# Optimization experiments

Hardware: AMD Instinct MI355X
Metric: run time of the kernel (lower is better)

The kernel has to match this reference:

```python
import jax, jax.numpy as jnp
import numpy as np

C_S, C_P, C_H, H, P_QK, P_V = 384, 128, 16, 12, 4, 8
B, N = 1, 512
INF = 1e5
EPS = 1e-8


def quat_to_rot(q):
    w, x, y, z = q[..., 0], q[..., 1], q[..., 2], q[..., 3]
    return jnp.stack([
        jnp.stack([1 - 2 * (y * y + z * z), 2 * (x * y - w * z), 2 * (x * z + w * y)], -1),
        jnp.stack([2 * (x * y + w * z), 1 - 2 * (x * x + z * z), 2 * (y * z - w * x)], -1),
        jnp.stack([2 * (x * z - w * y), 2 * (y * z + w * x), 1 - 2 * (x * x + y * y)], -1),
    ], -2)


def layer_norm(x, g, b):
    m = x.mean(-1, keepdims=True)
    v = ((x - m) ** 2).mean(-1, keepdims=True)
    return (x - m) * jax.lax.rsqrt(v + 1e-5) * g + b


def setup_inputs():
    key = jax.random.key(0)
    ks = iter(jax.random.split(key, 64))

    def w(shape, scale=0.02):
        return jax.random.normal(next(ks), shape, dtype=jnp.float32) * scale

    inp = {}
    inp['s'] = jax.random.normal(next(ks), (B, N, C_S), dtype=jnp.float32)
    inp['p'] = jax.random.normal(next(ks), (B, N, N, C_P), dtype=jnp.float32)
    q = jax.random.normal(next(ks), (B, N, 4), dtype=jnp.float32)
    inp['rot'] = quat_to_rot(q / jnp.linalg.norm(q, axis=-1, keepdims=True))
    inp['trans'] = jax.random.normal(next(ks), (B, N, 3), dtype=jnp.float32)
    inp['mask'] = jnp.ones((B, N), dtype=jnp.float32)
    inp['w_q'] = w((C_S, H * C_H)); inp['b_q'] = jnp.zeros((H * C_H,), jnp.float32)
    inp['w_kv'] = w((C_S, 2 * H * C_H)); inp['b_kv'] = jnp.zeros((2 * H * C_H,), jnp.float32)
    inp['w_qp'] = w((C_S, H * P_QK * 3)); inp['b_qp'] = jnp.zeros((H * P_QK * 3,), jnp.float32)
    inp['w_kvp'] = w((C_S, H * (P_QK + P_V) * 3)); inp['b_kvp'] = jnp.zeros((H * (P_QK + P_V) * 3,), jnp.float32)
    inp['w_b'] = w((C_P, H)); inp['b_b'] = jnp.zeros((H,), jnp.float32)
    inp['head_w'] = w((H,), 0.5)
    d_out = H * (C_H + C_P + P_V * 4)  # 2112
    inp['w_o'] = w((d_out, C_S)); inp['b_o'] = jnp.zeros((C_S,), jnp.float32)
    inp['ln1_g'] = jnp.ones((C_S,), jnp.float32); inp['ln1_b'] = jnp.zeros((C_S,), jnp.float32)
    for i in (1, 2, 3):
        inp['tw%d' % i] = w((C_S, C_S)); inp['tb%d' % i] = jnp.zeros((C_S,), jnp.float32)
    inp['ln2_g'] = jnp.ones((C_S,), jnp.float32); inp['ln2_b'] = jnp.zeros((C_S,), jnp.float32)
    inp['bb_w'] = w((C_S, 6)); inp['bb_b'] = jnp.zeros((6,), jnp.float32)
    return inp


def forward(s, p, rot, trans, mask, w_q, b_q, w_kv, b_kv, w_qp, b_qp, w_kvp, b_kvp,
            w_b, b_b, head_w, w_o, b_o, ln1_g, ln1_b,
            tw1, tb1, tw2, tb2, tw3, tb3, ln2_g, ln2_b, bb_w, bb_b):
    # ---- Invariant Point Attention ----
    q = (s @ w_q + b_q).reshape(B, N, H, C_H)
    k, v = jnp.split((s @ w_kv + b_kv).reshape(B, N, H, 2 * C_H), 2, axis=-1)
    qp = (s @ w_qp + b_qp).reshape(B, N, H * P_QK, 3)
    qp = (jnp.einsum('bnij,bnpj->bnpi', rot, qp) + trans[:, :, None, :]).reshape(B, N, H, P_QK, 3)
    kvp = (s @ w_kvp + b_kvp).reshape(B, N, H * (P_QK + P_V), 3)
    kvp = (jnp.einsum('bnij,bnpj->bnpi', rot, kvp) + trans[:, :, None, :]).reshape(B, N, H, P_QK + P_V, 3)
    kp, vp = kvp[..., :P_QK, :], kvp[..., P_QK:, :]
    bias = p @ w_b + b_b  # [B,N,N,H]
    a = jnp.einsum('bihc,bjhc->bhij', q, k) * float(np.sqrt(1.0 / (3 * C_H)))
    a = a + float(np.sqrt(1.0 / 3)) * jnp.transpose(bias, (0, 3, 1, 2))
    d2 = ((qp[:, :, None] - kp[:, None]) ** 2).sum(-1)  # [B,N,N,H,Pqk]
    hw = jax.nn.softplus(head_w) * float(np.sqrt(1.0 / (3 * (P_QK * 9.0 / 2))))
    pt_att = -0.5 * (d2 * hw[:, None]).sum(-1)  # [B,N,N,H]
    sq_mask = (mask[:, :, None] * mask[:, None, :] - 1.0) * INF  # [B,N,N]
    a = jax.nn.softmax(a + jnp.transpose(pt_att, (0, 3, 1, 2)) + sq_mask[:, None], axis=-1)
    o = jnp.einsum('bhij,bjhc->bihc', a, v).reshape(B, N, H * C_H)
    op = jnp.einsum('bhij,bjhpc->bihpc', a, vp) - trans[:, :, None, None, :]
    op = jnp.einsum('bnji,bnhpj->bnhpi', rot, op)  # invert-apply frames
    op_norm = jnp.sqrt((op ** 2).sum(-1) + EPS)  # [B,N,H,Pv]
    o_pair = jnp.einsum('bhij,bijc->bihc', a, p).reshape(B, N, H * C_P)
    cat = jnp.concatenate([o, op.reshape(B, N, H * P_V * 3), op_norm.reshape(B, N, H * P_V), o_pair], -1)
    s = s + cat @ w_o + b_o
    s = layer_norm(s, ln1_g, ln1_b)
    # ---- structure transition (1 layer, residual + LN) ----
    h = jax.nn.relu(s @ tw1 + tb1)
    h = jax.nn.relu(h @ tw2 + tb2)
    s = layer_norm(s + h @ tw3 + tb3, ln2_g, ln2_b)
    # ---- backbone update + frame compose ----
    upd = s @ bb_w + bb_b  # [B,N,6]
    quat = jnp.concatenate([jnp.ones((B, N, 1), s.dtype), upd[..., :3]], -1)
    quat = quat / jnp.linalg.norm(quat, axis=-1, keepdims=True)
    r_u = quat_to_rot(quat)
    rot_new = jnp.einsum('bnij,bnjk->bnik', rot, r_u)
    trans_new = jnp.einsum('bnij,bnj->bni', rot, upd[..., 3:]) + trans
    return s, rot_new, trans_new


def reference(s, p, rot, trans, mask, w_q, b_q, w_kv, b_kv, w_qp, b_qp, w_kvp, b_kvp,
              w_b, b_b, head_w, w_o, b_o, ln1_g, ln1_b,
              tw1, tb1, tw2, tb2, tw3, tb3, ln2_g, ln2_b, bb_w, bb_b):
    return forward(s, p, rot, trans, mask, w_q, b_q, w_kv, b_kv, w_qp, b_qp, w_kvp, b_kvp,
                   w_b, b_b, head_w, w_o, b_o, ln1_g, ln1_b,
                   tw1, tb1, tw2, tb2, tw3, tb3, ln2_g, ln2_b, bb_w, bb_b)
```

## Files before the change

### kernel.cpp

```cpp
#include <hip/hip_runtime.h>
#include <math.h>

#define N 512
#define CS 384
#define CP 128
#define CH 16
#define NH 12
#define NN (N*N)
#define DCAT 2112
#define INFV 100000.0f

__device__ __constant__ float SC_QK = 0.14433756729740643f;
#define SC_B  0.57735026918962576f
#define HW_SC 0.13608276348795434f

typedef __attribute__((ext_vector_type(8))) short bf16x8;
typedef __attribute__((ext_vector_type(4))) float f32x4;
typedef __attribute__((ext_vector_type(4))) short sh4;
typedef __attribute__((ext_vector_type(4))) unsigned u32x4;
typedef unsigned short ushort_t;

__device__ inline short f2bf(float v) {
    unsigned u = __builtin_bit_cast(unsigned, v);
    u += 0x7FFF + ((u >> 16) & 1);
    return (short)(u >> 16);
}
__device__ inline float bf2f(ushort_t u) {
    unsigned x = ((unsigned)u) << 16;
    return __builtin_bit_cast(float, x);
}
__device__ __forceinline__ unsigned cvtpk(float a, float b) {
    unsigned r;
    asm("v_cvt_pk_bf16_f32 %0, %1, %2" : "=v"(r) : "v"(a), "v"(b));
    return r;
}

__device__ __forceinline__ void gload16(const void* g, void* l) {
    __builtin_amdgcn_global_load_lds(
        (const __attribute__((address_space(1))) unsigned int*)g,
        (__attribute__((address_space(3))) unsigned int*)l,
        16, 0, 0);
}

struct FrontArgs {
    const float* wsrc0; const float* wsrc1; const float* wsrc2; const float* wsrc3;
    const float* wsrc4; const float* wsrc5; const float* wsrc6; const float* wsrc7;
    ushort_t* wdst0; ushort_t* wdst1; ushort_t* wdst2; ushort_t* wdst3;
    ushort_t* wdst4; ushort_t* wdst5; ushort_t* wdst6; ushort_t* wdst7;
    const float* s; ushort_t* sbf;
    const float* bq; const float* bkv; const float* bqp; const float* bkvp;
    float* biasp;
    const float* p; const float* w_b; const float* b_b; ushort_t* bias_b;
};

__global__ __launch_bounds__(256) void front_kernel(FrontArgs a)
{
    __shared__ __align__(16) char SM[36864];
    const int b = blockIdx.x;
    const int t = threadIdx.x;
    if (b < 4096) {
        float* Pf = (float*)SM;
        ushort_t* Wbs = (ushort_t*)(SM + 32768);
        const int w = t >> 6;
        const size_t row0 = (size_t)b * 64;

        for (int idx = t; idx < 2048; idx += 256) {
            int h = idx >> 7, c = idx & 127;
            float v = (h < 12) ? a.w_b[c * 12 + h] : 0.f;
            int byte = h * 256 + ((c * 2) ^ ((h & 7) << 4));
            *(ushort_t*)((char*)Wbs + byte) = (ushort_t)f2bf(v);
        }
        #pragma unroll
        for (int k = 0; k < 8; ++k) {
            int s2 = k * 256 + t;
            int row = s2 >> 5, ch = s2 & 31;
            const char* src = (const char*)(a.p + (row0 + row) * 128) + ((ch ^ (row & 7)) * 16);
            gload16(src, (char*)Pf + (size_t)(k * 256 + w * 64) * 16);
        }
        __syncthreads();

        const int l = t & 63, lr = l & 15, hk = l >> 4;
        const int jb = w * 16;
        f32x4 acc = (f32x4){0.f, 0.f, 0.f, 0.f};
        #pragma unroll
        for (int ks = 0; ks < 4; ++ks) {
            int row = jb + lr;
            int kc = ks * 8 + hk * 2;
            const char* base = (const char*)Pf + row * 512;
            f32x4 v0 = *(const f32x4*)(base + ((kc ^ (row & 7)) * 16));
            f32x4 v1 = *(const f32x4*)(base + (((kc + 1) ^ (row & 7)) * 16));
            bf16x8 afr;
            afr[0] = f2bf(v0[0]); afr[1] = f2bf(v0[1]); afr[2] = f2bf(v0[2]); afr[3] = f2bf(v0[3]);
            afr[4] = f2bf(v1[0]); afr[5] = f2bf(v1[1]); afr[6] = f2bf(v1[2]); afr[7] = f2bf(v1[3]);
            bf16x8 bfr = *(const bf16x8*)((char*)Wbs + lr * 256 +
                            ((ks * 64 + hk * 16) ^ ((lr & 7) << 4)));
            acc = __builtin_amdgcn_mfma_f32_16x16x32_bf16(afr, bfr, acc, 0, 0, 0);
        }
        if (lr < 12) {
            float bb = a.b_b[lr];
            size_t gj = row0 + jb + hk * 4;
            sh4 o;
            #pragma unroll
            for (int r = 0; r < 4; ++r) o[r] = f2bf(SC_B * (acc[r] + bb));
            *(sh4*)(a.bias_b + (size_t)lr * NN + gj) = o;
        }
    } else {
        const int bp = b - 4096;
        if (bp < 1668) {
            const float* src; ushort_t* dst; int begin, nx, Nc, K;
            if      (bp < 72)   { src=a.wsrc0; dst=a.wdst0; begin=0;    nx=6;  Nc=192; K=384; }
            else if (bp < 216)  { src=a.wsrc1; dst=a.wdst1; begin=72;   nx=12; Nc=384; K=384; }
            else if (bp < 276)  { src=a.wsrc2; dst=a.wdst2; begin=216;  nx=5;  Nc=144; K=384; }
            else if (bp < 444)  { src=a.wsrc3; dst=a.wdst3; begin=276;  nx=14; Nc=432; K=384; }
            else if (bp < 1236) { src=a.wsrc4; dst=a.wdst4; begin=444;  nx=12; Nc=384; K=2112; }
            else if (bp < 1380) { src=a.wsrc5; dst=a.wdst5; begin=1236; nx=12; Nc=384; K=384; }
            else if (bp < 1524) { src=a.wsrc6; dst=a.wdst6; begin=1380; nx=12; Nc=384; K=384; }
            else                { src=a.wsrc7; dst=a.wdst7; begin=1524; nx=12; Nc=384; K=384; }
            int lb = bp - begin;
            int cx = (lb % nx) * 32, ky = (lb / nx) * 32;
            float (*tile)[33] = (float(*)[33])SM;
            const int tx = t & 31, ty = t >> 5;
            for (int r = ty; r < 32; r += 8) {
                int c = cx + tx;
                tile[r][tx] = (c < Nc) ? src[(size_t)(ky + r) * Nc + c] : 0.f;
            }
            __syncthreads();
            for (int r = ty; r < 32; r += 8) {
                int orow = cx + r;
                if (orow < Nc)
                    dst[(size_t)orow * K + ky + tx] = (ushort_t)f2bf(tile[tx][r]);
            }
        } else if (bp < 1860) {
            int i4 = (bp - 1668) * 256 + t;
            f32x4 v = *(const f32x4*)(a.s + (size_t)i4 * 4);
            sh4 o;
            o[0] = f2bf(v[0]); o[1] = f2bf(v[1]); o[2] = f2bf(v[2]); o[3] = f2bf(v[3]);
            *(sh4*)(a.sbf + (size_t)i4 * 4) = o;
        } else {
            for (int idx = t; idx < 1152; idx += 256) {
                float v;
                if (idx < 192)      v = a.bq[idx];
                else if (idx < 576) v = a.bkv[idx - 192];
                else if (idx < 720) v = a.bqp[idx - 576];
                else                v = a.bkvp[idx - 720];
                a.biasp[idx] = v;
            }
        }
    }
}

__global__ __launch_bounds__(256) void gemm_bf16(
    const ushort_t* __restrict__ A, const ushort_t* __restrict__ Bt,
    float* __restrict__ part, int K, int KOUT, int nk)
{
    __shared__ __align__(16) ushort_t As[2][2048];
    __shared__ __align__(16) ushort_t Bs[2][2048];
    const int t = threadIdx.x, w = t >> 6, l = t & 63;
    const int i0 = blockIdx.x * 64, n0 = blockIdx.y * 64, sp = blockIdx.z;
    const int kbase = sp * nk * 32;

    const int srow = w * 16 + (l >> 2);
    const int skb = (l & 3) ^ ((srow >> 1) & 3);
    const ushort_t* aSrc = A + (size_t)(i0 + srow) * K + kbase + skb * 8;
    const ushort_t* bSrc = Bt + (size_t)(n0 + srow) * K + kbase + skb * 8;
    ushort_t* aDst = &As[0][0] + w * 512;
    ushort_t* bDst = &Bs[0][0] + w * 512;

    const int r0 = (w >> 1) * 32, c0 = (w & 1) * 32, lr = l & 15, hk = l >> 4;
    int aOff[2], bOff[2];
    #pragma unroll
    for (int m = 0; m < 2; ++m) {
        int row = r0 + m * 16 + lr;
        aOff[m] = row * 64 + ((hk ^ ((row >> 1) & 3)) << 4);
    }
    #pragma unroll
    for (int n = 0; n < 2; ++n) {
        int row = c0 + n * 16 + lr;
        bOff[n] = row * 64 + ((hk ^ ((row >> 1) & 3)) << 4);
    }

    f32x4 acc[2][2];
    #pragma unroll
    for (int m = 0; m < 2; ++m)
        #pragma unroll
        for (int n = 0; n < 2; ++n) acc[m][n] = (f32x4){0.f, 0.f, 0.f, 0.f};

    gload16(aSrc, aDst);
    gload16(bSrc, bDst);
    __syncthreads();

    int cur = 0;
    for (int it = 0; it < nk; ++it) {
        if (it + 1 < nk) {
            gload16(aSrc + (it + 1) * 32, aDst + (cur ^ 1) * 2048);
            gload16(bSrc + (it + 1) * 32, bDst + (cur ^ 1) * 2048);
        }
        const char* ab = (const char*)&As[cur][0];
        const char* bb = (const char*)&Bs[cur][0];
        bf16x8 a0 = *(const bf16x8*)(ab + aOff[0]);
// ... 207 lines not shown
    __shared__ float buf[1152];
    __shared__ float hwv[12], kc28[12];
    const int j = blockIdx.x, t = threadIdx.x;
    for (int c = t; c < 1152; c += 256)
        buf[c] = biasp[c] + parts[(size_t)j * 1152 + c] + parts[(size_t)(512 + j) * 1152 + c];
    if (t >= 192 && t < 204) {
        int h = t - 192;
        hwv[h] = HW_SC * log1pf(expf(head_w[h]));
    }
    __syncthreads();
    if (t < 192) {
        int base = 576 + t * 3;
        const float* R = rot + j * 9;
        const float* T = trans + j * 3;
        float x = buf[base], y = buf[base + 1], z = buf[base + 2];
        float nx = R[0]*x + R[1]*y + R[2]*z + T[0];
        float ny = R[3]*x + R[4]*y + R[5]*z + T[1];
        float nz = R[6]*x + R[7]*y + R[8]*z + T[2];
        buf[base] = nx; buf[base + 1] = ny; buf[base + 2] = nz;
    }
    __syncthreads();
    if (t < 12) {
        float s2 = 0.f;
        #pragma unroll
        for (int e = 0; e < 12; ++e) { float v = buf[720 + t * 36 + e]; s2 += v * v; }
        kc28[t] = -0.5f * hwv[t] * s2 + (mask[j] - 1.0f) * INFV;
    }
    __syncthreads();
    if (t < 192) {
        int h = t >> 4, c0 = (t & 15) * 2;
        float hwf = hwv[h];
        #pragma unroll
        for (int e = 0; e < 2; ++e) {
            int c = c0 + e;
            float qv, kv2;
            if (c < 16)      { qv = SC_QK * buf[h * 16 + c];           kv2 = buf[192 + h * 32 + c]; }
            else if (c < 28) { qv = hwf * buf[576 + h * 12 + (c - 16)]; kv2 = buf[720 + h * 36 + (c - 16)]; }
            else if (c == 28){ qv = 1.f;                               kv2 = kc28[h]; }
            else             { qv = 0.f;                               kv2 = 0.f; }
            Qext[(size_t)h * 16384 + j * 32 + c] = (ushort_t)f2bf(qv);
            Kext[(size_t)h * 16384 + j * 32 + c] = (ushort_t)f2bf(kv2);
        }
    }
    for (int idx = t; idx < 576; idx += 256) {
        int h = idx / 48, c = idx % 48;
        float v;
        if (c < 16)      v = buf[192 + h * 32 + 16 + c];
        else if (c < 40) v = buf[720 + h * 36 + 12 + (c - 16)];
        else             v = 0.f;
        Vext[(size_t)h * 24576 + c * 512 + j] = (ushort_t)f2bf(v);
    }
}

__global__ __launch_bounds__(256) void attn_mfma(
    const ushort_t* __restrict__ Qext, const ushort_t* __restrict__ Kext,
    const ushort_t* __restrict__ bias_b, const ushort_t* __restrict__ Vext,
    const float* __restrict__ rot, const float* __restrict__ trans,
    ushort_t* __restrict__ attn_b, ushort_t* __restrict__ catb)
{
    __shared__ float sc[16 * 516];
    __shared__ float redm[64];
    __shared__ float invr[16];
    __shared__ float opl[16][25];
    const int t = threadIdx.x, w = t >> 6, l = t & 63;
    const int i0 = blockIdx.x * 16, h = blockIdx.y;
    const int lr = l & 15, hk = l >> 4;

    #pragma unroll
    for (int it = 0; it < 8; ++it) {
        int elem = (t + it * 256) * 4;
        int i = elem >> 9, j = elem & 511;
        sh4 raw = *(const sh4*)(bias_b + (size_t)h * NN + (size_t)(i0 + i) * 512 + j);
        f32x4 v;
        v[0] = bf2f((ushort_t)raw[0]); v[1] = bf2f((ushort_t)raw[1]);
        v[2] = bf2f((ushort_t)raw[2]); v[3] = bf2f((ushort_t)raw[3]);
        *(f32x4*)(sc + i * 516 + j) = v;
    }
    __syncthreads();

    bf16x8 a0 = *(const bf16x8*)(Qext + (size_t)h * 16384 + (i0 + lr) * 32 + hk * 8);
    f32x4 acc[8];
    #pragma unroll
    for (int n = 0; n < 8; ++n) {
        bf16x8 b = *(const bf16x8*)(Kext + (size_t)h * 16384 +
                                    (w * 128 + n * 16 + lr) * 32 + hk * 8);
        acc[n] = __builtin_amdgcn_mfma_f32_16x16x32_bf16(a0, b, (f32x4){0.f,0.f,0.f,0.f}, 0, 0, 0);
    }

    float rmax[4] = {-3.0e38f, -3.0e38f, -3.0e38f, -3.0e38f};
    #pragma unroll
    for (int n = 0; n < 8; ++n) {
        int col = w * 128 + n * 16 + lr;
        #pragma unroll
        for (int r = 0; r < 4; ++r) {
            int row = hk * 4 + r;
            float v = acc[n][r] + sc[row * 516 + col];
            sc[row * 516 + col] = v;
            rmax[r] = fmaxf(rmax[r], v);
        }
    }
    #pragma unroll
    for (int r = 0; r < 4; ++r) {
        float v = rmax[r];
        v = fmaxf(v, __shfl_xor(v, 1));
        v = fmaxf(v, __shfl_xor(v, 2));
        v = fmaxf(v, __shfl_xor(v, 4));
        v = fmaxf(v, __shfl_xor(v, 8));
        if (lr == 0) redm[w * 16 + hk * 4 + r] = v;
    }
    __syncthreads();

    {
        int row = t >> 4, g = t & 15;
        float mx = fmaxf(fmaxf(redm[row], redm[16 + row]),
                         fmaxf(redm[32 + row], redm[48 + row]));
        float sum = 0.f;
        float* sr = sc + row * 516;
        for (int c = g; c < 512; c += 16) {
            float e = expf(sr[c] - mx);
            sr[c] = e;
            sum += e;
        }
        sum += __shfl_xor(sum, 1);
        sum += __shfl_xor(sum, 2);
        sum += __shfl_xor(sum, 4);
        sum += __shfl_xor(sum, 8);
        if (g == 0) invr[row] = 1.0f / sum;
    }
    __syncthreads();

    #pragma unroll
    for (int it = 0; it < 8; ++it) {
        int elem = (t + it * 256) * 4;
        int i = elem >> 9, j = elem & 511;
        f32x4 v = *(const f32x4*)(sc + i * 516 + j);
        float iv = invr[i];
        sh4 o;
        o[0] = f2bf(v[0] * iv); o[1] = f2bf(v[1] * iv);
        o[2] = f2bf(v[2] * iv); o[3] = f2bf(v[3] * iv);
        *(sh4*)(attn_b + (size_t)h * NN + (size_t)(i0 + i) * 512 + j) = o;
    }

    f32x4 acc3[3];
    acc3[0] = (f32x4){0.f,0.f,0.f,0.f};
    acc3[1] = (f32x4){0.f,0.f,0.f,0.f};
    acc3[2] = (f32x4){0.f,0.f,0.f,0.f};
    const ushort_t* vbase = Vext + (size_t)h * 24576 + lr * 512 + hk * 8;
    #pragma unroll
    for (int kt = 0; kt < 16; ++kt) {
        const float* srow = sc + lr * 516 + kt * 32 + hk * 8;
        f32x4 x0 = *(const f32x4*)(srow);
        f32x4 x1 = *(const f32x4*)(srow + 4);
        u32x4 ap;
        ap[0] = cvtpk(x0[0], x0[1]); ap[1] = cvtpk(x0[2], x0[3]);
        ap[2] = cvtpk(x1[0], x1[1]); ap[3] = cvtpk(x1[2], x1[3]);
        bf16x8 af = __builtin_bit_cast(bf16x8, ap);
        #pragma unroll
        for (int n = 0; n < 3; ++n) {
            bf16x8 bf = *(const bf16x8*)(vbase + n * 16 * 512 + kt * 32);
            acc3[n] = __builtin_amdgcn_mfma_f32_16x16x32_bf16(af, bf, acc3[n], 0, 0, 0);
        }
    }
    #pragma unroll
    for (int n = 0; n < 3; ++n) {
        int c = n * 16 + lr;
        #pragma unroll
        for (int r = 0; r < 4; ++r) {
            int ri = hk * 4 + r;
            float val = acc3[n][r] * invr[ri];
            if (c < 16)
                catb[(size_t)(i0 + ri) * DCAT + h * 16 + c] = (ushort_t)f2bf(val);
            else if (c < 40)
                opl[ri][c - 16] = val;
        }
    }
    __syncthreads();
    if (t < 128) {
        int i16 = t >> 3, pv = t & 7;
        int i = i0 + i16;
        const float* T = trans + i * 3;
        const float* R = rot + i * 9;
        float x = opl[i16][pv * 3 + 0] - T[0];
        float y = opl[i16][pv * 3 + 1] - T[1];
        float z = opl[i16][pv * 3 + 2] - T[2];
        float rx = R[0] * x + R[3] * y + R[6] * z;
        float ry = R[1] * x + R[4] * y + R[7] * z;
        float rz = R[2] * x + R[5] * y + R[8] * z;
        float nm = sqrtf(rx * rx + ry * ry + rz * rz + 1e-8f);
        ushort_t* cr = catb + (size_t)i * DCAT;
        cr[192 + h * 24 + pv * 3 + 0] = (ushort_t)f2bf(rx);
        cr[192 + h * 24 + pv * 3 + 1] = (ushort_t)f2bf(ry);
        cr[192 + h * 24 + pv * 3 + 2] = (ushort_t)f2bf(rz);
        cr[480 + h * 8 + pv] = (ushort_t)f2bf(nm);
    }
}

__global__ __launch_bounds__(256) void opair_mfma(
    const ushort_t* __restrict__ attn_b, const float* __restrict__ p,
    ushort_t* __restrict__ catb)
{
    __shared__ __align__(16) ushort_t As2[16 * 512];
    __shared__ __align__(16) ushort_t Pt[2][128 * 72];
    const int t = threadIdx.x, i = blockIdx.x;
    const int w = t >> 6, l = t & 63;
    const int lr = l & 15, hk = l >> 4;

    #pragma unroll
    for (int ii = 0; ii < 4; ++ii) {
        int idx = (t + ii * 256) * 8;
        int h = idx >> 9, j = idx & 511;
        bf16x8 v;
        if (h < 12) v = *(const bf16x8*)(attn_b + (size_t)h * NN + (size_t)i * 512 + j);
        else        v = (bf16x8){0,0,0,0,0,0,0,0};
        *(bf16x8*)((char*)As2 + h * 1024 + ((j * 2) ^ ((h & 7) << 4))) = v;
    }

    const int jA = (t >> 3) * 2;
    const int c0 = (t & 7) * 16;
    const float* psrc = p + (size_t)i * 65536;

    f32x4 va[4], vb[4];
    #pragma unroll
    for (int q = 0; q < 4; ++q) {
        va[q] = *(const f32x4*)(psrc + (size_t)jA * 128 + c0 + q * 4);
        vb[q] = *(const f32x4*)(psrc + (size_t)(jA + 1) * 128 + c0 + q * 4);
    }

    #define PACK_TILE(buf)                                                       \
        {                                                                        \
            ushort_t* ptw = &Pt[buf][0];                                         \
            _Pragma("unroll")                                                    \
            for (int e = 0; e < 16; ++e) {                                       \
                int c = c0 + e;                                                  \
                unsigned pk = cvtpk(va[e >> 2][e & 3], vb[e >> 2][e & 3]);       \
                int byte = c * 144 + ((jA * 2) ^ (((c >> 4) & 7) << 4));         \
                *(unsigned*)((char*)ptw + byte) = pk;                            \
            }                                                                    \
        }
    #define LOAD_TILE(tile)                                                      \
        {                                                                        \
            const float* s0 = psrc + (size_t)((tile) * 64 + jA) * 128 + c0;      \
            _Pragma("unroll")                                                    \
            for (int q = 0; q < 4; ++q) {                                        \
                va[q] = *(const f32x4*)(s0 + q * 4);                             \
                vb[q] = *(const f32x4*)(s0 + 128 + q * 4);                       \
            }                                                                    \
        }

    PACK_TILE(0);
    LOAD_TILE(1);

    f32x4 acc[2];
    acc[0] = (f32x4){0.f, 0.f, 0.f, 0.f};
    acc[1] = (f32x4){0.f, 0.f, 0.f, 0.f};

    int cur = 0;
    for (int tile = 0; tile < 8; ++tile) {
        __syncthreads();
        const char* pt = (const char*)&Pt[cur][0];
        #pragma unroll
        for (int ks = 0; ks < 2; ++ks) {
            bf16x8 afr = *(const bf16x8*)((char*)As2 + lr * 1024 +
                            ((tile * 128 + ks * 64 + hk * 16) ^ ((lr & 7) << 4)));
            #pragma unroll
            for (int n = 0; n < 2; ++n) {
                int c = w * 32 + n * 16 + lr;
                bf16x8 bfr = *(const bf16x8*)(pt + c * 144 +
                                ((ks * 64 + hk * 16) ^ (((c >> 4) & 7) << 4)));
                acc[n] = __builtin_amdgcn_mfma_f32_16x16x32_bf16(afr, bfr, acc[n], 0, 0, 0);
            }
        }
        if (tile < 7) {
            PACK_TILE(cur ^ 1);
            if (tile < 6) LOAD_TILE(tile + 2);
            cur ^= 1;
        }
    }
    #undef PACK_TILE
    #undef LOAD_TILE
    #pragma unroll
    for (int n = 0; n < 2; ++n) {
        int c = w * 32 + n * 16 + lr;
        #pragma unroll
        for (int r = 0; r < 4; ++r) {
            int h = hk * 4 + r;
            if (h < 12)
                catb[(size_t)i * DCAT + 576 + h * 128 + c] = (ushort_t)f2bf(acc[n][r]);
        }
    }
}

extern "C" void kernel_launch(void* const* d_in, const int* in_sizes, int n_in,
                              void* d_out, int out_size, void* d_ws, size_t ws_size,
                              hipStream_t stream)
{
    const float* s      = (const float*)d_in[0];
    const float* p      = (const float*)d_in[1];
    const float* rot    = (const float*)d_in[2];
    const float* trans  = (const float*)d_in[3];
    const float* mask   = (const float*)d_in[4];
    const float* w_q    = (const float*)d_in[5];
    const float* b_q    = (const float*)d_in[6];
    const float* w_kv   = (const float*)d_in[7];
    const float* b_kv   = (const float*)d_in[8];
    const float* w_qp   = (const float*)d_in[9];
    const float* b_qp   = (const float*)d_in[10];
    const float* w_kvp  = (const float*)d_in[11];
    const float* b_kvp  = (const float*)d_in[12];
    const float* w_b    = (const float*)d_in[13];
    const float* b_b    = (const float*)d_in[14];
    const float* head_w = (const float*)d_in[15];
    const float* w_o    = (const float*)d_in[16];
    const float* b_o    = (const float*)d_in[17];
    const float* ln1_g  = (const float*)d_in[18];
    const float* ln1_b  = (const float*)d_in[19];
    const float* tw1    = (const float*)d_in[20];
    const float* tb1    = (const float*)d_in[21];
    const float* tw2    = (const float*)d_in[22];
    const float* tb2    = (const float*)d_in[23];
    const float* tw3    = (const float*)d_in[24];
    const float* tb3    = (const float*)d_in[25];
    const float* ln2_g  = (const float*)d_in[26];
    const float* ln2_b  = (const float*)d_in[27];
    const float* bb_w   = (const float*)d_in[28];
    const float* bb_b   = (const float*)d_in[29];

    float* ws = (float*)d_ws;
    float*    parts  = ws;
    float*    partsB = parts + 589824;
    float*    s1     = parts + 1179648;
    float*    biasp  = s1 + 196608;
    ushort_t* ub     = (ushort_t*)(biasp + 1152);
    ushort_t* bias_b = ub;
    ushort_t* attn_b = bias_b + 3145728;
    ushort_t* catb   = attn_b + 3145728;
    ushort_t* sbf    = catb + 1081344;
    ushort_t* s1bf   = sbf + 196608;
    ushort_t* h1bf   = s1bf + 196608;
    ushort_t* h2bf   = h1bf + 196608;
    ushort_t* Qext   = h2bf + 196608;
    ushort_t* Kext   = Qext + 196608;
    ushort_t* Vext   = Kext + 196608;
    ushort_t* Wtp    = Vext + 294912;
    ushort_t* Wto    = Wtp + 442368;
    ushort_t* Wt1    = Wto + 811008;
    ushort_t* Wt2    = Wt1 + 147456;
    ushort_t* Wt3    = Wt2 + 147456;

    float* out_s     = (float*)d_out;
    float* out_rot   = out_s + 196608;
    float* out_trans = out_rot + 4608;

    FrontArgs fa;
    fa.wsrc0 = w_q;  fa.wdst0 = Wtp;
    fa.wsrc1 = w_kv; fa.wdst1 = Wtp + (size_t)192 * 384;
    fa.wsrc2 = w_qp; fa.wdst2 = Wtp + (size_t)576 * 384;
    fa.wsrc3 = w_kvp; fa.wdst3 = Wtp + (size_t)720 * 384;
    fa.wsrc4 = w_o;  fa.wdst4 = Wto;
    fa.wsrc5 = tw1;  fa.wdst5 = Wt1;
    fa.wsrc6 = tw2;  fa.wdst6 = Wt2;
    fa.wsrc7 = tw3;  fa.wdst7 = Wt3;
    fa.s = s; fa.sbf = sbf;
    fa.bq = b_q; fa.bkv = b_kv; fa.bqp = b_qp; fa.bkvp = b_kvp;
    fa.biasp = biasp;
    fa.p = p; fa.w_b = w_b; fa.b_b = b_b; fa.bias_b = bias_b;
    front_kernel<<<5957, 256, 0, stream>>>(fa);

    gemm_bf16<<<dim3(8, 18, 2), 256, 0, stream>>>(sbf, Wtp, parts, 384, 1152, 6);
    postproj_kernel<<<512, 256, 0, stream>>>(parts, biasp, rot, trans, head_w, mask,
                                             Qext, Kext, Vext);

    attn_mfma<<<dim3(32, 12), 256, 0, stream>>>(Qext, Kext, bias_b, Vext, rot, trans,
                                                attn_b, catb);
    opair_mfma<<<512, 256, 0, stream>>>(attn_b, p, catb);

    gemm_bf16<<<dim3(8, 6, 6), 256, 0, stream>>>(catb, Wto, parts, 2112, 384, 11);
    reduce_ln<<<512, 128, 0, stream>>>(parts, 6, b_o, s, ln1_g, ln1_b, s1, s1bf,
                                       nullptr, nullptr, nullptr, nullptr, nullptr, nullptr);

    gemm_bf16<<<dim3(8, 6, 3), 256, 0, stream>>>(s1bf, Wt1, parts, 384, 384, 4);
    gemm_red<<<dim3(8, 6, 3), 256, 0, stream>>>(parts, tb1, Wt2, partsB, 4);
    gemm_red<<<dim3(8, 6, 3), 256, 0, stream>>>(partsB, tb2, Wt3, parts, 4);
    reduce_ln<<<512, 128, 0, stream>>>(parts, 3, tb3, s1, ln2_g, ln2_b, out_s, nullptr,
                                       bb_w, bb_b, rot, trans, out_rot, out_trans);
}
```

Measured before the change: 124.7 us.

## Fuse pair-bias projection, softmax, and pair-output into one pass over p

The pair tensor p used to be read twice: once in the front kernel to build the pair bias and once in the opair kernel for the output-pair product. A new per-row mega_attn kernel now loads each p tile once, computes the bias by MFMA, adds precomputed QK logits, runs an online softmax across 8 tiles, and accumulates the attention-weighted sum of p in the same pass. The QK logits are now computed by a separate small kernel and written head-interleaved, and the attention-times-V product moves into its own ov_mfma kernel. This roughly halves traffic on the large p tensor and drops the bf16 bias buffer, in exchange for more synchronisation per tile and an extra kernel launch.

```diff
diff --git a/kernel.cpp b/kernel.cpp
--- a/kernel.cpp
+++ b/kernel.cpp
@@ -42,7 +42,7 @@
         16, 0, 0);
 }
 
-struct FrontArgs {
+struct PrepArgs {
     const float* wsrc0; const float* wsrc1; const float* wsrc2; const float* wsrc3;
     const float* wsrc4; const float* wsrc5; const float* wsrc6; const float* wsrc7;
     ushort_t* wdst0; ushort_t* wdst1; ushort_t* wdst2; ushort_t* wdst3;
@@ -50,101 +50,50 @@
     const float* s; ushort_t* sbf;
     const float* bq; const float* bkv; const float* bqp; const float* bkvp;
     float* biasp;
-    const float* p; const float* w_b; const float* b_b; ushort_t* bias_b;
 };
 
-__global__ __launch_bounds__(256) void front_kernel(FrontArgs a)
-{
-    __shared__ __align__(16) char SM[36864];
-    const int b = blockIdx.x;
+__global__ __launch_bounds__(256) void prep_kernel(PrepArgs a)
+{
+    __shared__ float tile[32][33];
+    const int bp = blockIdx.x;
     const int t = threadIdx.x;
-    if (b < 4096) {
-        float* Pf = (float*)SM;
-        ushort_t* Wbs = (ushort_t*)(SM + 32768);
-        const int w = t >> 6;
-        const size_t row0 = (size_t)b * 64;
-
-        for (int idx = t; idx < 2048; idx += 256) {
-            int h = idx >> 7, c = idx & 127;
-            float v = (h < 12) ? a.w_b[c * 12 + h] : 0.f;
-            int byte = h * 256 + ((c * 2) ^ ((h & 7) << 4));
-            *(ushort_t*)((char*)Wbs + byte) = (ushort_t)f2bf(v);
-        }
-        #pragma unroll
-        for (int k = 0; k < 8; ++k) {
-            int s2 = k * 256 + t;
-            int row = s2 >> 5, ch = s2 & 31;
-            const char* src = (const char*)(a.p + (row0 + row) * 128) + ((ch ^ (row & 7)) * 16);
-            gload16(src, (char*)Pf + (size_t)(k * 256 + w * 64) * 16);
+    if (bp < 1668) {
+        const float* src; ushort_t* dst; int begin, nx, Nc, K;
+        if      (bp < 72)   { src=a.wsrc0; dst=a.wdst0; begin=0;    nx=6;  Nc=192; K=384; }
+        else if (bp < 216)  { src=a.wsrc1; dst=a.wdst1; begin=72;   nx=12; Nc=384; K=384; }
+        else if (bp < 276)  { src=a.wsrc2; dst=a.wdst2; begin=216;  nx=5;  Nc=144; K=384; }
+        else if (bp < 444)  { src=a.wsrc3; dst=a.wdst3; begin=276;  nx=14; Nc=432; K=384; }
+        else if (bp < 1236) { src=a.wsrc4; dst=a.wdst4; begin=444;  nx=12; Nc=384; K=2112; }
+        else if (bp < 1380) { src=a.wsrc5; dst=a.wdst5; begin=1236; nx=12; Nc=384; K=384; }
+        else if (bp < 1524) { src=a.wsrc6; dst=a.wdst6; begin=1380; nx=12; Nc=384; K=384; }
+        else                { src=a.wsrc7; dst=a.wdst7; begin=1524; nx=12; Nc=384; K=384; }
+        int lb = bp - begin;
+        int cx = (lb % nx) * 32, ky = (lb / nx) * 32;
+        const int tx = t & 31, ty = t >> 5;
+        for (int r = ty; r < 32; r += 8) {
+            int c = cx + tx;
+            tile[r][tx] = (c < Nc) ? src[(size_t)(ky + r) * Nc + c] : 0.f;
         }
         __syncthreads();
-
-        const int l = t & 63, lr = l & 15, hk = l >> 4;
-        const int jb = w * 16;
-        f32x4 acc = (f32x4){0.f, 0.f, 0.f, 0.f};
-        #pragma unroll
-        for (int ks = 0; ks < 4; ++ks) {
-            int row = jb + lr;
-            int kc = ks * 8 + hk * 2;
-            const char* base = (const char*)Pf + row * 512;
-            f32x4 v0 = *(const f32x4*)(base + ((kc ^ (row & 7)) * 16));
-            f32x4 v1 = *(const f32x4*)(base + (((kc + 1) ^ (row & 7)) * 16));
-            bf16x8 afr;
-            afr[0] = f2bf(v0[0]); afr[1] = f2bf(v0[1]); afr[2] = f2bf(v0[2]); afr[3] = f2bf(v0[3]);
-            afr[4] = f2bf(v1[0]); afr[5] = f2bf(v1[1]); afr[6] = f2bf(v1[2]); afr[7] = f2bf(v1[3]);
-            bf16x8 bfr = *(const bf16x8*)((char*)Wbs + lr * 256 +
-                            ((ks * 64 + hk * 16) ^ ((lr & 7) << 4)));
-            acc = __builtin_amdgcn_mfma_f32_16x16x32_bf16(afr, bfr, acc, 0, 0, 0);
-        }
-        if (lr < 12) {
-            float bb = a.b_b[lr];
-            size_t gj = row0 + jb + hk * 4;
-            sh4 o;
-            #pragma unroll
-            for (int r = 0; r < 4; ++r) o[r] = f2bf(SC_B * (acc[r] + bb));
-            *(sh4*)(a.bias_b + (size_t)lr * NN + gj) = o;
-        }
+        for (int r = ty; r < 32; r += 8) {
+            int orow = cx + r;
+            if (orow < Nc)
+                dst[(size_t)orow * K + ky + tx] = (ushort_t)f2bf(tile[tx][r]);
+        }
+    } else if (bp < 1860) {
+        int i4 = (bp - 1668) * 256 + t;
+        f32x4 v = *(const f32x4*)(a.s + (size_t)i4 * 4);
+        sh4 o;
+        o[0] = f2bf(v[0]); o[1] = f2bf(v[1]); o[2] = f2bf(v[2]); o[3] = f2bf(v[3]);
+        *(sh4*)(a.sbf + (size_t)i4 * 4) = o;
     } else {
-        const int bp = b - 4096;
-        if (bp < 1668) {
-            const float* src; ushort_t* dst; int begin, nx, Nc, K;
-            if      (bp < 72)   { src=a.wsrc0; dst=a.wdst0; begin=0;    nx=6;  Nc=192; K=384; }
-            else if (bp < 216)  { src=a.wsrc1; dst=a.wdst1; begin=72;   nx=12; Nc=384; K=384; }
-            else if (bp < 276)  { src=a.wsrc2; dst=a.wdst2; begin=216;  nx=5;  Nc=144; K=384; }
-            else if (bp < 444)  { src=a.wsrc3; dst=a.wdst3; begin=276;  nx=14; Nc=432; K=384; }
-            else if (bp < 1236) { src=a.wsrc4; dst=a.wdst4; begin=444;  nx=12; Nc=384; K=2112; }
-            else if (bp < 1380) { src=a.wsrc5; dst=a.wdst5; begin=1236; nx=12; Nc=384; K=384; }
-            else if (bp < 1524) { src=a.wsrc6; dst=a.wdst6; begin=1380; nx=12; Nc=384; K=384; }
-            else                { src=a.wsrc7; dst=a.wdst7; begin=1524; nx=12; Nc=384; K=384; }
-            int lb = bp - begin;
-            int cx = (lb % nx) * 32, ky = (lb / nx) * 32;
-            float (*tile)[33] = (float(*)[33])SM;
-            const int tx = t & 31, ty = t >> 5;
-            for (int r = ty; r < 32; r += 8) {
-                int c = cx + tx;
-                tile[r][tx] = (c < Nc) ? src[(size_t)(ky + r) * Nc + c] : 0.f;
-            }
-            __syncthreads();
-            for (int r = ty; r < 32; r += 8) {
-                int orow = cx + r;
-                if (orow < Nc)
-                    dst[(size_t)orow * K + ky + tx] = (ushort_t)f2bf(tile[tx][r]);
-            }
-        } else if (bp < 1860) {
-            int i4 = (bp - 1668) * 256 + t;
-            f32x4 v = *(const f32x4*)(a.s + (size_t)i4 * 4);
-            sh4 o;
-            o[0] = f2bf(v[0]); o[1] = f2bf(v[1]); o[2] = f2bf(v[2]); o[3] = f2bf(v[3]);
-            *(sh4*)(a.sbf + (size_t)i4 * 4) = o;
-        } else {
-            for (int idx = t; idx < 1152; idx += 256) {
-                float v;
-                if (idx < 192)      v = a.bq[idx];
-                else if (idx < 576) v = a.bkv[idx - 192];
-                else if (idx < 720) v = a.bqp[idx - 576];
-                else                v = a.bkvp[idx - 720];
-                a.biasp[idx] = v;
-            }
+        for (int idx = t; idx < 1152; idx += 256) {
+            float v;
+            if (idx < 192)      v = a.bq[idx];
+            else if (idx < 576) v = a.bkv[idx - 192];
+            else if (idx < 720) v = a.bqp[idx - 576];
+            else                v = a.bkvp[idx - 720];
+            a.biasp[idx] = v;
         }
     }
 }
@@ -458,113 +407,245 @@
     }
 }
 
-__global__ __launch_bounds__(256) void attn_mfma(
+__global__ __launch_bounds__(256) void qk_kernel(
     const ushort_t* __restrict__ Qext, const ushort_t* __restrict__ Kext,
-    const ushort_t* __restrict__ bias_b, const ushort_t* __restrict__ Vext,
-    const float* __restrict__ rot, const float* __restrict__ trans,
-    ushort_t* __restrict__ attn_b, ushort_t* __restrict__ catb)
-{
-    __shared__ float sc[16 * 516];
-    __shared__ float redm[64];
-    __shared__ float invr[16];
-    __shared__ float opl[16][25];
+    ushort_t* __restrict__ qk_b)
+{
     const int t = threadIdx.x, w = t >> 6, l = t & 63;
     const int i0 = blockIdx.x * 16, h = blockIdx.y;
     const int lr = l & 15, hk = l >> 4;
-
-    #pragma unroll
-    for (int it = 0; it < 8; ++it) {
-        int elem = (t + it * 256) * 4;
-        int i = elem >> 9, j = elem & 511;
-        sh4 raw = *(const sh4*)(bias_b + (size_t)h * NN + (size_t)(i0 + i) * 512 + j);
-        f32x4 v;
-        v[0] = bf2f((ushort_t)raw[0]); v[1] = bf2f((ushort_t)raw[1]);
-        v[2] = bf2f((ushort_t)raw[2]); v[3] = bf2f((ushort_t)raw[3]);
-        *(f32x4*)(sc + i * 516 + j) = v;
-    }
-    __syncthreads();
-
     bf16x8 a0 = *(const bf16x8*)(Qext + (size_t)h * 16384 + (i0 + lr) * 32 + hk * 8);
-    f32x4 acc[8];
     #pragma unroll
     for (int n = 0; n < 8; ++n) {
         bf16x8 b = *(const bf16x8*)(Kext + (size_t)h * 16384 +
                                     (w * 128 + n * 16 + lr) * 32 + hk * 8);
-        acc[n] = __builtin_amdgcn_mfma_f32_16x16x32_bf16(a0, b, (f32x4){0.f,0.f,0.f,0.f}, 0, 0, 0);
-    }
-
-    float rmax[4] = {-3.0e38f, -3.0e38f, -3.0e38f, -3.0e38f};
-    #pragma unroll
-    for (int n = 0; n < 8; ++n) {
-        int col = w * 128 + n * 16 + lr;
+        f32x4 acc = __builtin_amdgcn_mfma_f32_16x16x32_bf16(
+                        a0, b, (f32x4){0.f, 0.f, 0.f, 0.f}, 0, 0, 0);
+        int j = w * 128 + n * 16 + lr;
         #pragma unroll
         for (int r = 0; r < 4; ++r) {
-            int row = hk * 4 + r;
-            float v = acc[n][r] + sc[row * 516 + col];
-            sc[row * 516 + col] = v;
-            rmax[r] = fmaxf(rmax[r], v);
-        }
-    }
-    #pragma unroll
-    for (int r = 0; r < 4; ++r) {
-        float v = rmax[r];
-        v = fmaxf(v, __shfl_xor(v, 1));
-        v = fmaxf(v, __shfl_xor(v, 2));
-        v = fmaxf(v, __shfl_xor(v, 4));
-        v = fmaxf(v, __shfl_xor(v, 8));
-        if (lr == 0) redm[w * 16 + hk * 4 + r] = v;
-    }
-    __syncthreads();
-
+            int i = i0 + hk * 4 + r;
+            qk_b[((size_t)i * 512 + j) * 16 + h] = (ushort_t)f2bf(acc[r]);
+        }
+    }
+}
+
+__global__ __launch_bounds__(256) void mega_attn(
+    const float* __restrict__ p, const ushort_t* __restrict__ qk_b,
+    const float* __restrict__ w_b, const float* __restrict__ b_b,
+    ushort_t* __restrict__ attn_b, ushort_t* __restrict__ catb)
+{
+    __shared__ __align__(16) ushort_t Wbs[16 * 128];
+    __shared__ __align__(16) ushort_t Pr[64 * 128];
+    __shared__ __align__(16) ushort_t Pt[128 * 72];
+    __shared__ __align__(16) ushort_t qkT[64 * 16];
+    __shared__ __align__(16) ushort_t wT[16 * 64];
+    __shared__ __align__(16) ushort_t wFull[16 * 512];
+    __shared__ float mTile[16][8];
+    __shared__ float redw[4][16], redw2[4][16];
+    __shared__ float fArr[16], lArr[16], mArr[16];
+
+    const int t = threadIdx.x, i = blockIdx.x;
+    const int w = t >> 6, l = t & 63, lr = l & 15, hk = l >> 4;
+
+    for (int idx = t; idx < 2048; idx += 256) {
+        int h = idx >> 7, c = idx & 127;
+        float v = (h < 12) ? SC_B * w_b[c * 12 + h] : 0.f;
+        *(ushort_t*)((char*)Wbs + h * 256 + ((c * 2) ^ ((h & 7) << 4))) = (ushort_t)f2bf(v);
+    }
+    const float sc_bb = (lr < 12) ? SC_B * b_b[lr] : 0.f;
+
+    const float* psrc = p + (size_t)i * 65536;
+    const int jA = (t >> 3) * 2, c0 = (t & 7) * 16;
+
+    f32x4 va[4], vb[4];
+    #define LOAD_REGS(tile)                                                      \
+        {                                                                        \
+            const float* s0 = psrc + (size_t)((tile) * 64 + jA) * 128 + c0;      \
+            _Pragma("unroll")                                                    \
+            for (int q = 0; q < 4; ++q) {                                        \
+                va[q] = *(const f32x4*)(s0 + q * 4);                             \
+                vb[q] = *(const f32x4*)(s0 + 128 + q * 4);                       \
+            }                                                                    \
+        }
+    #define WRITE_BUFS()                                                         \
+        {                                                                        \
+            _Pragma("unroll")                                                    \
+            for (int r2 = 0; r2 < 2; ++r2) {                                     \
+                int j = jA + r2;                                                 \
+                const f32x4* vr = r2 ? vb : va;                                  \
+                _Pragma("unroll")                                                \
+                for (int half = 0; half < 2; ++half) {                           \
+                    u32x4 pk;                                                    \
+                    pk[0] = cvtpk(vr[half*2][0], vr[half*2][1]);                 \
+                    pk[1] = cvtpk(vr[half*2][2], vr[half*2][3]);                 \
+                    pk[2] = cvtpk(vr[half*2+1][0], vr[half*2+1][1]);             \
+                    pk[3] = cvtpk(vr[half*2+1][2], vr[half*2+1][3]);             \
+                    int byte = j * 256 + (((c0 + half * 8) * 2) ^ ((j & 7) << 4));\
+                    *(u32x4*)((char*)Pr + byte) = pk;                            \
+                }                                                                \
+            }                                                                    \
+            _Pragma("unroll")                                                    \
+            for (int e = 0; e < 16; ++e) {                                       \
+                int c = c0 + e;                                                  \
+                unsigned pk = cvtpk(va[e >> 2][e & 3], vb[e >> 2][e & 3]);       \
+                int byte = c * 144 + ((jA * 2) ^ (((c >> 4) & 7) << 4));         \
+                *(unsigned*)((char*)Pt + byte) = pk;                             \
+            }                                                                    \
+        }
+    #define STAGE_QK(tile)                                                      \
+        if (t < 128)                                                            \
+            gload16(qk_b + ((size_t)i * 512 + (tile) * 64) * 16 + t * 8,        \
+                    (char*)qkT + t * 16);
+
+    LOAD_REGS(0);
+    STAGE_QK(0);
+    __syncthreads();
+    WRITE_BUFS();
+    LOAD_REGS(1);
+    float m_reg = -3.0e38f, l_reg = 0.f;
+    f32x4 accP[2];
+    accP[0] = (f32x4){0.f, 0.f, 0.f, 0.f};
+    accP[1] = (f32x4){0.f, 0.f, 0.f, 0.f};
+    __syncthreads();
+
+    const int jl2 = w * 16 + lr;
+    for (int tile = 0; tile < 8; ++tile) {
+        f32x4 S = (f32x4){0.f, 0.f, 0.f, 0.f};
+        #pragma unroll
+        for (int ks = 0; ks < 4; ++ks) {
+            bf16x8 afr = *(const bf16x8*)((char*)Pr + jl2 * 256 +
+                            ((ks * 64 + hk * 16) ^ ((jl2 & 7) << 4)));
+            bf16x8 bfr = *(const bf16x8*)((char*)Wbs + lr * 256 +
+                            ((ks * 64 + hk * 16) ^ ((lr & 7) << 4)));
+            S = __builtin_amdgcn_mfma_f32_16x16x32_bf16(afr, bfr, S, 0, 0, 0);
+        }
+        float sv[4];
+        float tmax = -3.0e38f;
+        #pragma unroll
+        for (int r = 0; r < 4; ++r) {
+            int jloc = w * 16 + hk * 4 + r;
+            float qkv = (lr < 12) ? bf2f(qkT[jloc * 16 + lr]) : 0.f;
+            sv[r] = S[r] + sc_bb + qkv;
+            tmax = fmaxf(tmax, sv[r]);
+        }
+        tmax = fmaxf(tmax, __shfl_xor(tmax, 16));
+        tmax = fmaxf(tmax, __shfl_xor(tmax, 32));
+        if (hk == 0) redw[w][lr] = tmax;
+        __syncthreads();
+        if (tile < 7) STAGE_QK(tile + 1);
+        float mt = fmaxf(fmaxf(redw[0][lr], redw[1][lr]),
+                         fmaxf(redw[2][lr], redw[3][lr]));
+        float m_new = fmaxf(m_reg, mt);
+        float f = __expf(m_reg - m_new);
+        m_reg = m_new;
+        float tsum = 0.f;
+        ushort_t wv16[4];
+        #pragma unroll
+        for (int r = 0; r < 4; ++r) {
+            float wv = __expf(sv[r] - m_new);
+            tsum += wv;
+            wv16[r] = (ushort_t)f2bf(wv);
+        }
+        tsum += __shfl_xor(tsum, 16);
+        tsum += __shfl_xor(tsum, 32);
+        if (hk == 0) redw2[w][lr] = tsum;
+        if (w == 0 && hk == 0) { fArr[lr] = f; mTile[lr][tile] = m_new; }
+        #pragma unroll
+        for (int r = 0; r < 4; ++r) {
+            int j = w * 16 + hk * 4 + r;
+            *(ushort_t*)((char*)wT + lr * 128 + ((j * 2) ^ ((lr & 7) << 4))) = wv16[r];
+            int jg = tile * 64 + j;
+            *(ushort_t*)((char*)wFull + lr * 1024 + ((jg * 2) ^ ((lr & 7) << 4))) = wv16[r];
+        }
+        __syncthreads();
+        float sumAll = redw2[0][lr] + redw2[1][lr] + redw2[2][lr] + redw2[3][lr];
+        l_reg = l_reg * f + sumAll;
+        #pragma unroll
+        for (int n = 0; n < 2; ++n)
+            #pragma unroll
+            for (int r = 0; r < 4; ++r) accP[n][r] *= fArr[hk * 4 + r];
+        #pragma unroll
+        for (int ks = 0; ks < 2; ++ks) {
+            bf16x8 afr = *(const bf16x8*)((char*)wT + lr * 128 +
+                            ((ks * 64 + hk * 16) ^ ((lr & 7) << 4)));
+            #pragma unroll
+            for (int n = 0; n < 2; ++n) {
+                int c = w * 32 + n * 16 + lr;
+                bf16x8 bfr = *(const bf16x8*)((char*)Pt + c * 144 +
+                                ((ks * 64 + hk * 16) ^ (((c >> 4) & 7) << 4)));
+                accP[n] = __builtin_amdgcn_mfma_f32_16x16x32_bf16(afr, bfr, accP[n], 0, 0, 0);
+            }
+        }
+        __syncthreads();
+        if (tile < 7) {
+            WRITE_BUFS();
+            if (tile < 6) LOAD_REGS(tile + 2);
+        }
+        __syncthreads();
+    }
+    #undef LOAD_REGS
+    #undef WRITE_BUFS
+    #undef STAGE_QK
+
+    if (w == 0 && hk == 0) { lArr[lr] = l_reg; mArr[lr] = m_reg; }
+    __syncthreads();
+
+    #pragma unroll
+    for (int n = 0; n < 2; ++n) {
+        int c = w * 32 + n * 16 + lr;
+        #pragma unroll
+        for (int r = 0; r < 4; ++r) {
+            int h = hk * 4 + r;
+            if (h < 12)
+                catb[(size_t)i * DCAT + 576 + h * 128 + c] =
+                    (ushort_t)f2bf(accP[n][r] / lArr[h]);
+        }
+    }
     {
-        int row = t >> 4, g = t & 15;
-        float mx = fmaxf(fmaxf(redm[row], redm[16 + row]),
-                         fmaxf(redm[32 + row], redm[48 + row]));
-        float sum = 0.f;
-        float* sr = sc + row * 516;
-        for (int c = g; c < 512; c += 16) {
-            float e = expf(sr[c] - mx);
-            sr[c] = e;
-            sum += e;
-        }
-        sum += __shfl_xor(sum, 1);
-        sum += __shfl_xor(sum, 2);
-        sum += __shfl_xor(sum, 4);
-        sum += __shfl_xor(sum, 8);
-        if (g == 0) invr[row] = 1.0f / sum;
-    }
-    __syncthreads();
-
-    #pragma unroll
-    for (int it = 0; it < 8; ++it) {
-        int elem = (t + it * 256) * 4;
-        int i = elem >> 9, j = elem & 511;
-        f32x4 v = *(const f32x4*)(sc + i * 516 + j);
-        float iv = invr[i];
-        sh4 o;
-        o[0] = f2bf(v[0] * iv); o[1] = f2bf(v[1] * iv);
-        o[2] = f2bf(v[2] * iv); o[3] = f2bf(v[3] * iv);
-        *(sh4*)(attn_b + (size_t)h * NN + (size_t)(i0 + i) * 512 + j) = o;
-    }
-
-    f32x4 acc3[3];
-    acc3[0] = (f32x4){0.f,0.f,0.f,0.f};
-    acc3[1] = (f32x4){0.f,0.f,0.f,0.f};
-    acc3[2] = (f32x4){0.f,0.f,0.f,0.f};
+        int h = t >> 4;
+        if (h < 12) {
+            float linv = 1.0f / lArr[h];
+            float mfin = mArr[h];
+            #pragma unroll
+            for (int e = 0; e < 4; ++e) {
+                int cp = (t & 15) * 4 + e;
+                int jc = cp ^ (h & 7);
+                int j0 = jc * 8;
+                float corr = __expf(mTile[h][j0 >> 6] - mfin) * linv;
+                bf16x8 raw = *(const bf16x8*)((char*)wFull + h * 1024 + cp * 16);
+                bf16x8 o;
+                #pragma unroll
+                for (int q = 0; q < 8; ++q)
+                    o[q] = (short)f2bf(bf2f((ushort_t)raw[q]) * corr);
+                *(bf16x8*)(attn_b + (size_t)h * NN + (size_t)i * 512 + j0) = o;
+            }
+        }
+    }
+}
+
+__global__ __launch_bounds__(64) void ov_mfma(
+    const ushort_t* __restrict__ attn_b, const ushort_t* __restrict__ Vext,
+    const float* __restrict__ rot, const float* __restrict__ trans,
+    ushort_t* __restrict__ catb)
+{
+    __shared__ float opl[16][25];
+    const int l = threadIdx.x;
+    const int i0 = blockIdx.x * 16, h = blockIdx.y;
+    const int lr = l & 15, hk = l >> 4;
+    f32x4 acc[3];
+    acc[0] = (f32x4){0.f,0.f,0.f,0.f};
+    acc[1] = (f32x4){0.f,0.f,0.f,0.f};
+    acc[2] = (f32x4){0.f,0.f,0.f,0.f};
+    const ushort_t* arow = attn_b + (size_t)h * NN + (size_t)(i0 + lr) * 512 + hk * 8;
     const ushort_t* vbase = Vext + (size_t)h * 24576 + lr * 512 + hk * 8;
     #pragma unroll
     for (int kt = 0; kt < 16; ++kt) {
-        const float* srow = sc + lr * 516 + kt * 32 + hk * 8;
-        f32x4 x0 = *(const f32x4*)(srow);
-        f32x4 x1 = *(const f32x4*)(srow + 4);
-        u32x4 ap;
-        ap[0] = cvtpk(x0[0], x0[1]); ap[1] = cvtpk(x0[2], x0[3]);
-        ap[2] = cvtpk(x1[0], x1[1]); ap[3] = cvtpk(x1[2], x1[3]);
-        bf16x8 af = __builtin_bit_cast(bf16x8, ap);
+        bf16x8 af = *(const bf16x8*)(arow + kt * 32);
         #pragma unroll
         for (int n = 0; n < 3; ++n) {
             bf16x8 bf = *(const bf16x8*)(vbase + n * 16 * 512 + kt * 32);
-            acc3[n] = __builtin_amdgcn_mfma_f32_16x16x32_bf16(af, bf, acc3[n], 0, 0, 0);
+            acc[n] = __builtin_amdgcn_mfma_f32_16x16x32_bf16(af, bf, acc[n], 0, 0, 0);
         }
     }
     #pragma unroll
@@ -573,16 +654,17 @@
         #pragma unroll
         for (int r = 0; r < 4; ++r) {
             int ri = hk * 4 + r;
-            float val = acc3[n][r] * invr[ri];
             if (c < 16)
-                catb[(size_t)(i0 + ri) * DCAT + h * 16 + c] = (ushort_t)f2bf(val);
+                catb[(size_t)(i0 + ri) * DCAT + h * 16 + c] = (ushort_t)f2bf(acc[n][r]);
             else if (c < 40)
-                opl[ri][c - 16] = val;
-        }
-    }
-    __syncthreads();
-    if (t < 128) {
-        int i16 = t >> 3, pv = t & 7;
+                opl[ri][c - 16] = acc[n][r];
+        }
+    }
+    __syncthreads();
+    #pragma unroll
+    for (int e = 0; e < 2; ++e) {
+        int pt = l + e * 64;
+        int i16 = pt >> 3, pv = pt & 7;
         int i = i0 + i16;
         const float* T = trans + i * 3;
         const float* R = rot + i * 9;
@@ -598,101 +680,6 @@
         cr[192 + h * 24 + pv * 3 + 1] = (ushort_t)f2bf(ry);
         cr[192 + h * 24 + pv * 3 + 2] = (ushort_t)f2bf(rz);
         cr[480 + h * 8 + pv] = (ushort_t)f2bf(nm);
-    }
-}
-
-__global__ __launch_bounds__(256) void opair_mfma(
-    const ushort_t* __restrict__ attn_b, const float* __restrict__ p,
-    ushort_t* __restrict__ catb)
-{
-    __shared__ __align__(16) ushort_t As2[16 * 512];
-    __shared__ __align__(16) ushort_t Pt[2][128 * 72];
-    const int t = threadIdx.x, i = blockIdx.x;
-    const int w = t >> 6, l = t & 63;
-    const int lr = l & 15, hk = l >> 4;
-
-    #pragma unroll
-    for (int ii = 0; ii < 4; ++ii) {
-        int idx = (t + ii * 256) * 8;
-        int h = idx >> 9, j = idx & 511;
-        bf16x8 v;
-        if (h < 12) v = *(const bf16x8*)(attn_b + (size_t)h * NN + (size_t)i * 512 + j);
-        else        v = (bf16x8){0,0,0,0,0,0,0,0};
-        *(bf16x8*)((char*)As2 + h * 1024 + ((j * 2) ^ ((h & 7) << 4))) = v;
-    }
-
-    const int jA = (t >> 3) * 2;
-    const int c0 = (t & 7) * 16;
-    const float* psrc = p + (size_t)i * 65536;
-
-    f32x4 va[4], vb[4];
-    #pragma unroll
-    for (int q = 0; q < 4; ++q) {
-        va[q] = *(const f32x4*)(psrc + (size_t)jA * 128 + c0 + q * 4);
-        vb[q] = *(const f32x4*)(psrc + (size_t)(jA + 1) * 128 + c0 + q * 4);
-    }
-
-    #define PACK_TILE(buf)                                                       \
-        {                                                                        \
-            ushort_t* ptw = &Pt[buf][0];                                         \
-            _Pragma("unroll")                                                    \
-            for (int e = 0; e < 16; ++e) {                                       \
-                int c = c0 + e;                                                  \
-                unsigned pk = cvtpk(va[e >> 2][e & 3], vb[e >> 2][e & 3]);       \
-                int byte = c * 144 + ((jA * 2) ^ (((c >> 4) & 7) << 4));         \
-                *(unsigned*)((char*)ptw + byte) = pk;                            \
-            }                                                                    \
-        }
-    #define LOAD_TILE(tile)                                                      \
-        {                                                                        \
-            const float* s0 = psrc + (size_t)((tile) * 64 + jA) * 128 + c0;      \
-            _Pragma("unroll")                                                    \
-            for (int q = 0; q < 4; ++q) {                                        \
-                va[q] = *(const f32x4*)(s0 + q * 4);                             \
-                vb[q] = *(const f32x4*)(s0 + 128 + q * 4);                       \
-            }                                                                    \
-        }
-
-    PACK_TILE(0);
-    LOAD_TILE(1);
-
-    f32x4 acc[2];
-    acc[0] = (f32x4){0.f, 0.f, 0.f, 0.f};
-    acc[1] = (f32x4){0.f, 0.f, 0.f, 0.f};
-
-    int cur = 0;
-    for (int tile = 0; tile < 8; ++tile) {
-        __syncthreads();
-        const char* pt = (const char*)&Pt[cur][0];
-        #pragma unroll
-        for (int ks = 0; ks < 2; ++ks) {
-            bf16x8 afr = *(const bf16x8*)((char*)As2 + lr * 1024 +
-                            ((tile * 128 + ks * 64 + hk * 16) ^ ((lr & 7) << 4)));
-            #pragma unroll
-            for (int n = 0; n < 2; ++n) {
-                int c = w * 32 + n * 16 + lr;
-                bf16x8 bfr = *(const bf16x8*)(pt + c * 144 +
-                                ((ks * 64 + hk * 16) ^ (((c >> 4) & 7) << 4)));
-                acc[n] = __builtin_amdgcn_mfma_f32_16x16x32_bf16(afr, bfr, acc[n], 0, 0, 0);
-            }
-        }
-        if (tile < 7) {
-            PACK_TILE(cur ^ 1);
-            if (tile < 6) LOAD_TILE(tile + 2);
-            cur ^= 1;
-        }
-    }
-    #undef PACK_TILE
-    #undef LOAD_TILE
-    #pragma unroll
-    for (int n = 0; n < 2; ++n) {
-        int c = w * 32 + n * 16 + lr;
-        #pragma unroll
-        for (int r = 0; r < 4; ++r) {
-            int h = hk * 4 + r;
-            if (h < 12)
-                catb[(size_t)i * DCAT + 576 + h * 128 + c] = (ushort_t)f2bf(acc[n][r]);
-        }
     }
 }
 
@@ -737,14 +724,11 @@
     float*    s1     = parts + 1179648;
     float*    biasp  = s1 + 196608;
     ushort_t* ub     = (ushort_t*)(biasp + 1152);
-    ushort_t* bias_b = ub;
-    ushort_t* attn_b = bias_b + 3145728;
+    ushort_t* attn_b = ub;
     ushort_t* catb   = attn_b + 3145728;
     ushort_t* sbf    = catb + 1081344;
     ushort_t* s1bf   = sbf + 196608;
-    ushort_t* h1bf   = s1bf + 196608;
-    ushort_t* h2bf   = h1bf + 196608;
-    ushort_t* Qext   = h2bf + 196608;
+    ushort_t* Qext   = s1bf + 196608;
     ushort_t* Kext   = Qext + 196608;
     ushort_t* Vext   = Kext + 196608;
     ushort_t* Wtp    = Vext + 294912;
@@ -752,33 +736,33 @@
     ushort_t* Wt1    = Wto + 811008;
     ushort_t* Wt2    = Wt1 + 147456;
     ushort_t* Wt3    = Wt2 + 147456;
+    ushort_t* qk_b   = Wt3 + 147456;
 
     float* out_s     = (float*)d_out;
     float* out_rot   = out_s + 196608;
     float* out_trans = out_rot + 4608;
 
-    FrontArgs fa;
-    fa.wsrc0 = w_q;  fa.wdst0 = Wtp;
-    fa.wsrc1 = w_kv; fa.wdst1 = Wtp + (size_t)192 * 384;
-    fa.wsrc2 = w_qp; fa.wdst2 = Wtp + (size_t)576 * 384;
-    fa.wsrc3 = w_kvp; fa.wdst3 = Wtp + (size_t)720 * 384;
-    fa.wsrc4 = w_o;  fa.wdst4 = Wto;
-    fa.wsrc5 = tw1;  fa.wdst5 = Wt1;
-    fa.wsrc6 = tw2;  fa.wdst6 = Wt2;
-    fa.wsrc7 = tw3;  fa.wdst7 = Wt3;
-    fa.s = s; fa.sbf = sbf;
-    fa.bq = b_q; fa.bkv = b_kv; fa.bqp = b_qp; fa.bkvp = b_kvp;
-    fa.biasp = biasp;
-    fa.p = p; fa.w_b = w_b; fa.b_b = b_b; fa.bias_b = bias_b;
-    front_kernel<<<5957, 256, 0, stream>>>(fa);
+    PrepArgs pa;
+    pa.wsrc0 = w_q;  pa.wdst0 = Wtp;
+    pa.wsrc1 = w_kv; pa.wdst1 = Wtp + (size_t)192 * 384;
+    pa.wsrc2 = w_qp; pa.wdst2 = Wtp + (size_t)576 * 384;
+    pa.wsrc3 = w_kvp; pa.wdst3 = Wtp + (size_t)720 * 384;
+    pa.wsrc4 = w_o;  pa.wdst4 = Wto;
+    pa.wsrc5 = tw1;  pa.wdst5 = Wt1;
+    pa.wsrc6 = tw2;  pa.wdst6 = Wt2;
+    pa.wsrc7 = tw3;  pa.wdst7 = Wt3;
+    pa.s = s; pa.sbf = sbf;
+    pa.bq = b_q; pa.bkv = b_kv; pa.bqp = b_qp; pa.bkvp = b_kvp;
+    pa.biasp = biasp;
+    prep_kernel<<<1861, 256, 0, stream>>>(pa);
 
     gemm_bf16<<<dim3(8, 18, 2), 256, 0, stream>>>(sbf, Wtp, parts, 384, 1152, 6);
     postproj_kernel<<<512, 256, 0, stream>>>(parts, biasp, rot, trans, head_w, mask,
                                              Qext, Kext, Vext);
 
-    attn_mfma<<<dim3(32, 12), 256, 0, stream>>>(Qext, Kext, bias_b, Vext, rot, trans,
-                                                attn_b, catb);
-    opair_mfma<<<512, 256, 0, stream>>>(attn_b, p, catb);
+    qk_kernel<<<dim3(32, 12), 256, 0, stream>>>(Qext, Kext, qk_b);
+    mega_attn<<<512, 256, 0, stream>>>(p, qk_b, w_b, b_b, attn_b, catb);
+    ov_mfma<<<dim3(32, 12), 64, 0, stream>>>(attn_b, Vext, rot, trans, catb);
 
     gemm_bf16<<<dim3(8, 6, 6), 256, 0, stream>>>(catb, Wto, parts, 2112, 384, 11);
     reduce_ln<<<512, 128, 0, stream>>>(parts, 6, b_o, s, ln1_g, ln1_b, s1, s1bf,
```

Result: faster. 105.8 us (-15.2%).
